# Optimization experiments

Measured on AMD Instinct MI355X. Metric: run time of the kernel, lower is better.

## Reference

```python
import jax, jax.numpy as jnp
import numpy as np

_SAMPLING_EPS = 1e-5
EOS_PROB_RATIO = 100.0
MIN_PROB_THRESHOLD = 0.001
MIX_RATIO = 0.5
EOS_TOKEN_ID = 2


def setup_inputs() -> dict:
    key = jax.random.key(0)
    k1, k2, k3, k4 = jax.random.split(key, 4)
    B, V = 256, 128000
    logits = jax.random.normal(k1, (B, V), dtype=jnp.float32) * 3.0
    # keep temperature away from 0 so the random-sampling path is exercised
    temperature = 0.2 + 1.3 * jax.random.uniform(k2, (B,), dtype=jnp.float32)
    top_p = 0.5 + 0.5 * jax.random.uniform(k3, (B,), dtype=jnp.float32)
    token_lengths = jax.random.randint(k4, (V,), 0, 20).astype(jnp.int32)
    return {
        "logits": logits,
        "temperature": temperature,
        "top_p": top_p,
        "token_lengths": token_lengths,
        "top_k": 50,
    }


def _apply_top_k_top_p(logits, top_k, top_p):
    """vLLM-style: ascending sort, top-k threshold, top-p cumulative mask, scatter back."""
    idx = jnp.argsort(logits, axis=-1)  # ascending
    lsort = jnp.take_along_axis(logits, idx, axis=-1)
    V = logits.shape[-1]
    # top-k: keep only the last top_k (largest) entries
    kth = lsort[:, V - top_k][:, None]
    lsort = jnp.where(lsort < kth, -jnp.inf, lsort)
    # top-p: mask low-cumulative-probability prefix (ascending order)
    probs = jax.nn.softmax(lsort, axis=-1)
    csum = jnp.cumsum(probs, axis=-1)
    pmask = csum <= (1.0 - top_p[:, None])
    pmask = pmask.at[:, -1].set(False)  # always keep the top token
    lsort = jnp.where(pmask, -jnp.inf, lsort)
    # scatter back to original token order
    inv = jnp.argsort(idx, axis=-1)
    return jnp.take_along_axis(lsort, inv, axis=-1)


def _longest_word_sample(logits, token_lengths, k, mix_ratio, eos_token_id):
    topk_logits, topk_idx = jax.lax.top_k(logits, k)  # [B,k]
    prob = jax.nn.softmax(topk_logits, axis=-1)
    lens = token_lengths[jnp.clip(topk_idx, 0, token_lengths.shape[0] - 1)].astype(jnp.float32)
    length_score = jax.nn.softmax(lens, axis=-1)
    mix = (1.0 - mix_ratio) * prob + mix_ratio * length_score
    mix = jnp.where(prob >= MIN_PROB_THRESHOLD, mix, -jnp.inf)
    # EOS threshold rule
    eos_in_topk = (topk_idx == eos_token_id) & jnp.isfinite(topk_logits)
    rows_with_eos = eos_in_topk.any(axis=-1, keepdims=True)
    eos_prob = jnp.sum(prob * eos_in_topk, axis=-1, keepdims=True)
    eos_thresh = jnp.maximum(eos_prob / EOS_PROB_RATIO, 0.005)
    valid = prob >= eos_thresh
    mix = jnp.where(valid | ~rows_with_eos, mix, -jnp.inf)
    best = jnp.argmax(mix, axis=-1)  # [B]
    chosen = jnp.take_along_axis(topk_idx, best[:, None], axis=-1)[:, 0]
    return chosen


def reference(logits, temperature, top_p, token_lengths, top_k):
    greedy = jnp.argmax(logits, axis=-1)
    scaled = logits / temperature[:, None]
    filtered = _apply_top_k_top_p(scaled, top_k, top_p)
    rnd = _longest_word_sample(filtered, token_lengths, top_k, MIX_RATIO, EOS_TOKEN_ID)
    sampled = jnp.where(temperature < _SAMPLING_EPS, greedy, rnd)
    return sampled.astype(jnp.int32)
```

## Files before the change

### kernel.cpp

```cpp
#include <hip/hip_runtime.h>
#include <stdint.h>
#include <math.h>

#define THREADS 1024
#define NWAVES 16
#define NBINS 8192
#define BIN_SHIFT 19
#define CAND_MAX 1536
#define MAXK 64
#define RING 4

__device__ __forceinline__ uint32_t fkey(float f) {
    uint32_t b = __float_as_uint(f);
    return (b & 0x80000000u) ? ~b : (b | 0x80000000u);
}
__device__ __forceinline__ float fval(uint32_t k) {
    uint32_t b = (k & 0x80000000u) ? (k & 0x7FFFFFFFu) : ~k;
    return __uint_as_float(b);
}

__device__ __forceinline__ void gload_lds16(const float* g, uint32_t* lds) {
    __builtin_amdgcn_global_load_lds(
        (const __attribute__((address_space(1))) void*)(const void*)g,
        (__attribute__((address_space(3))) void*)(void*)lds,
        16, 0, 0);
}

__global__ __launch_bounds__(THREADS, 1) void sampler_kernel(
    const float* __restrict__ logits,
    const float* __restrict__ temperature,
    const float* __restrict__ top_p,
    const int* __restrict__ token_lengths,
    const int* __restrict__ top_k_ptr,
    int* __restrict__ out, int V)
{
    const int row  = blockIdx.x;
    const int tid  = threadIdx.x;
    const int lane = tid & 63;
    const int wid  = tid >> 6;
    int K = *top_k_ptr;
    if (K < 1) K = 1;
    if (K > MAXK) K = MAXK;

    __shared__ __align__(16) uint32_t s_stage[NWAVES * RING * 256];
    __shared__ uint32_t s_hist[NBINS];
    __shared__ unsigned long long s_cand[CAND_MAX];
    __shared__ uint32_t s_wsum[NWAVES], s_wtail[NWAVES];
    __shared__ float s_vals[MAXK];
    __shared__ int s_idx[MAXK], s_slot[MAXK];
    __shared__ int s_T, s_cnt;

    for (int i = tid; i < NBINS; i += THREADS) s_hist[i] = 0u;
    if (tid == 0) s_cnt = 0;
    __syncthreads();

    const float* rowbase = logits + (size_t)row * (size_t)V;
    const int NREAL = (V + 255) >> 8;
    const int NITER = (NREAL + NWAVES - 1) / NWAVES;
    const int lastg = V - 4;
    uint32_t* mystage = &s_stage[wid * (RING * 256)];

    #pragma unroll
    for (int k = 0; k < RING - 1; ++k) {
        int ci = wid + NWAVES * k;
        int c  = (ci < NREAL - 1) ? ci : (NREAL - 1);
        int g  = c * 256 + lane * 4;
        g = (g < lastg) ? g : lastg;
        gload_lds16(rowbase + g, mystage + k * 256);
    }
    for (int i = 0; i < NITER; ++i) {
        asm volatile("s_waitcnt vmcnt(2)" ::: "memory");
        const uint32_t* sp = mystage + (i & (RING - 1)) * 256 + lane * 4;
        float4 x = *reinterpret_cast<const float4*>(sp);
        const int g0 = (wid + NWAVES * i) * 256 + lane * 4;
        if (g0 < V) {
            atomicAdd(&s_hist[fkey(x.x) >> BIN_SHIFT], 1u);
            atomicAdd(&s_hist[fkey(x.y) >> BIN_SHIFT], 1u);
            atomicAdd(&s_hist[fkey(x.z) >> BIN_SHIFT], 1u);
            atomicAdd(&s_hist[fkey(x.w) >> BIN_SHIFT], 1u);
        }
        {
            int ci = wid + NWAVES * (i + RING - 1);
            int c  = (ci < NREAL - 1) ? ci : (NREAL - 1);
            int g  = c * 256 + lane * 4;
            g = (g < lastg) ? g : lastg;
            gload_lds16(rowbase + g, mystage + ((i + RING - 1) & (RING - 1)) * 256);
        }
    }
    asm volatile("s_waitcnt vmcnt(0)" ::: "memory");
    __syncthreads();

    const int CH = NBINS / THREADS;
    uint32_t cs = 0;
    {
        const int b0 = tid * CH;
        #pragma unroll
        for (int b = 0; b < CH; ++b) cs += s_hist[b0 + b];
    }
    uint32_t suf = cs;
    #pragma unroll
    for (int off = 1; off < 64; off <<= 1) {
        uint32_t o = __shfl_down(suf, off, 64);
        suf += (lane + off < 64) ? o : 0u;
    }
    if (lane == 0) s_wsum[wid] = suf;
    __syncthreads();
    if (wid == 0 && lane < NWAVES) {
        uint32_t t = s_wsum[lane];
        uint32_t s = t;
        #pragma unroll
        for (int off = 1; off < NWAVES; off <<= 1) {
            uint32_t o = __shfl_down(s, off, 64);
            s += (lane + off < NWAVES) ? o : 0u;
        }
        s_wtail[lane] = s - t;
    }
    __syncthreads();
    {
        uint32_t sufg = suf + s_wtail[wid];
        uint32_t sufn = sufg - cs;
        if (sufg >= (uint32_t)K && sufn < (uint32_t)K) {
            uint32_t acc = sufn;
            int T = tid * CH;
            for (int b = tid * CH + CH - 1; b >= tid * CH; --b) {
                acc += s_hist[b];
                if (acc >= (uint32_t)K) { T = b; break; }
            }
            s_T = T;
        }
    }
    __syncthreads();

    const uint32_t T = (uint32_t)s_T;
    #pragma unroll
    for (int k = 0; k < RING - 1; ++k) {
        int ci = wid + NWAVES * k;
        int c  = (ci < NREAL - 1) ? ci : (NREAL - 1);
        int g  = c * 256 + lane * 4;
        g = (g < lastg) ? g : lastg;
        gload_lds16(rowbase + g, mystage + k * 256);
    }
    for (int i = 0; i < NITER; ++i) {
        asm volatile("s_waitcnt vmcnt(2)" ::: "memory");
        const uint32_t* sp = mystage + (i & (RING - 1)) * 256 + lane * 4;
        float4 x = *reinterpret_cast<const float4*>(sp);
        const int g0 = (wid + NWAVES * i) * 256 + lane * 4;
        if (g0 < V) {
            uint32_t k0;
            k0 = fkey(x.x); if ((k0 >> BIN_SHIFT) >= T) { int p = atomicAdd(&s_cnt, 1); if (p < CAND_MAX) s_cand[p] = ((unsigned long long)k0 << 32) | (uint32_t)~(uint32_t)(g0 + 0); }
            k0 = fkey(x.y); if ((k0 >> BIN_SHIFT) >= T) { int p = atomicAdd(&s_cnt, 1); if (p < CAND_MAX) s_cand[p] = ((unsigned long long)k0 << 32) | (uint32_t)~(uint32_t)(g0 + 1); }
            k0 = fkey(x.z); if ((k0 >> BIN_SHIFT) >= T) { int p = atomicAdd(&s_cnt, 1); if (p < CAND_MAX) s_cand[p] = ((unsigned long long)k0 << 32) | (uint32_t)~(uint32_t)(g0 + 2); }
            k0 = fkey(x.w); if ((k0 >> BIN_SHIFT) >= T) { int p = atomicAdd(&s_cnt, 1); if (p < CAND_MAX) s_cand[p] = ((unsigned long long)k0 << 32) | (uint32_t)~(uint32_t)(g0 + 3); }
        }
        {
            int ci = wid + NWAVES * (i + RING - 1);
            int c  = (ci < NREAL - 1) ? ci : (NREAL - 1);
            int g  = c * 256 + lane * 4;
            g = (g < lastg) ? g : lastg;
            gload_lds16(rowbase + g, mystage + ((i + RING - 1) & (RING - 1)) * 256);
        }
    }
    asm volatile("s_waitcnt vmcnt(0)" ::: "memory");
    __syncthreads();

    const int M = (s_cnt < CAND_MAX) ? s_cnt : CAND_MAX;
    for (int t = tid; t < M; t += THREADS) {
        const unsigned long long mine = s_cand[t];
        int rank = 0;
        for (int j = 0; j < M; ++j) rank += (s_cand[j] > mine) ? 1 : 0;
        if (rank < MAXK) {
            s_idx[rank]  = (int)(~(uint32_t)mine);
            s_vals[rank] = fval((uint32_t)(mine >> 32));
        }
    }
    __syncthreads();

    if (tid >= 64) return;

    const float temp = temperature[row];
    const float tp   = top_p[row];

    const float a0 = s_vals[0] / temp;
    float e = 0.f;
    int myidx = -1;
    if (tid < K) {
        myidx = s_idx[tid];
        e = expf(s_vals[tid] / temp - a0);
    }
    float sum = e;
    #pragma unroll
    for (int off = 1; off < 64; off <<= 1) sum += __shfl_xor(sum, off, 64);
    const float p1 = e / sum;

    float csf = p1;
    #pragma unroll
    for (int off = 1; off < 64; off <<= 1) {
        float o = __shfl_down(csf, off, 64);
        csf += (tid + off < 64) ? o : 0.f;
    }
    const float lim = 1.0f - tp;
    const bool keep = (tid < K) && (tid == 0 || csf > lim);
    const int S = __popcll(__ballot(keep));

    float e2 = (tid < S) ? e : 0.f;
    float sum2 = e2;
    #pragma unroll
    for (int off = 1; off < 64; off <<= 1) sum2 += __shfl_xor(sum2, off, 64);
    const float p2 = e2 / sum2;

    const bool is_eos = (tid < S) && (myidx == 2);
    float eosp = is_eos ? p2 : 0.f;
    #pragma unroll
    for (int off = 1; off < 64; off <<= 1) eosp += __shfl_xor(eosp, off, 64);
    const bool has_eos = (__ballot(is_eos) != 0ull);
    const float eth = fmaxf(eosp / 100.0f, 0.005f);

    if (tid < S) s_slot[tid] = myidx;
    __builtin_amdgcn_wave_barrier();
    if (tid == 0) {
        unsigned long long m0 = 0ull, m1 = 0ull;
        for (int i = 0; i < S; ++i) {
            int id = s_idx[i];
            if (id < 64) m0 |= 1ull << id;
            else if (id < 128) m1 |= 1ull << (id - 64);
        }
        int nxt = 0;
        for (int i = S; i < K; ++i) {
            while ((nxt < 64) ? ((m0 >> nxt) & 1ull) : ((m1 >> (nxt - 64)) & 1ull)) nxt++;
            s_slot[i] = nxt++;
        }
    }
    __builtin_amdgcn_wave_barrier();

    float len = -INFINITY;
    if (tid < K) {
        int id = s_slot[tid];
        id = (id < 0) ? 0 : ((id >= V) ? V - 1 : id);
        len = (float)token_lengths[id];
    }
    float lmax = len;
    #pragma unroll
    for (int off = 1; off < 64; off <<= 1) lmax = fmaxf(lmax, __shfl_xor(lmax, off, 64));
    float el = (tid < K) ? expf(len - lmax) : 0.f;
    float lsum = el;
    #pragma unroll
    for (int off = 1; off < 64; off <<= 1) lsum += __shfl_xor(lsum, off, 64);
    const float ls = el / lsum;

    float mix = -INFINITY;
    if (tid < S) {
        mix = 0.5f * p2 + 0.5f * ls;
        if (!(p2 >= 0.001f)) mix = -INFINITY;
        if (has_eos && !(p2 >= eth)) mix = -INFINITY;
    }
    float bm = mix; int bi = tid;
    #pragma unroll
    for (int off = 1; off < 64; off <<= 1) {
        float om = __shfl_xor(bm, off, 64);
        int   oi = __shfl_xor(bi, off, 64);
        if (om > bm || (om == bm && oi < bi)) { bm = om; bi = oi; }
    }

    if (tid == 0) {
        int chosen = s_slot[bi];
        if (temp < 1e-5f) chosen = s_idx[0];
        out[row] = chosen;
    }
}

extern "C" void kernel_launch(void* const* d_in, const int* in_sizes, int n_in,
                              void* d_out, int out_size, void* d_ws, size_t ws_size,
                              hipStream_t stream) {
    const float* logits        = (const float*)d_in[0];
    const float* temperature   = (const float*)d_in[1];
    const float* top_p         = (const float*)d_in[2];
    const int*   token_lengths = (const int*)d_in[3];
    const int*   top_k_ptr     = (const int*)d_in[4];
    int* outp = (int*)d_out;

    const int B = in_sizes[1];
    const int V = in_sizes[3];

    sampler_kernel<<<B, THREADS, 0, stream>>>(logits, temperature, top_p,
                                              token_lengths, top_k_ptr, outp, V);
}
```

Before: 51.55 us.

## Replace two-pass histogram top-k with single-pass per-thread top-4 plus fallback

Each thread now streams its slice of the row once with batched float4 register loads and keeps a running top-4 (packed key plus index), plus the largest value it discarded. The histogram and candidate selection then work on only 4096 per-thread survivors instead of rescanning the full row. A check compares the discarded maxima against the K-th result and, if any thread dropped a qualifying element, falls back to a full rescan of the row. This removes the second full pass over global memory and the per-element LDS atomics, at the cost of per-element register insertion work and a rare slow path.

```diff
diff --git a/kernel.cpp b/kernel.cpp
--- a/kernel.cpp
+++ b/kernel.cpp
@@ -6,9 +6,9 @@
 #define NWAVES 16
 #define NBINS 8192
 #define BIN_SHIFT 19
-#define CAND_MAX 1536
+#define CAND_MAX 1024
 #define MAXK 64
-#define RING 4
+#define BATCH 16
 
 __device__ __forceinline__ uint32_t fkey(float f) {
     uint32_t b = __float_as_uint(f);
@@ -19,12 +19,19 @@
     return __uint_as_float(b);
 }
 
-__device__ __forceinline__ void gload_lds16(const float* g, uint32_t* lds) {
-    __builtin_amdgcn_global_load_lds(
-        (const __attribute__((address_space(1))) void*)(const void*)g,
-        (__attribute__((address_space(3))) void*)(void*)lds,
-        16, 0, 0);
-}
+#define INS(vf, gidx) do {                                                       \
+    unsigned long long p_ = ((unsigned long long)fkey(vf) << 32)                 \
+                          | (uint32_t)~(uint32_t)(gidx);                         \
+    if (p_ > t3) {                                                               \
+        dmax = (t3 > dmax) ? t3 : dmax;                                          \
+        t3 = p_;                                                                 \
+        if (t3 > t2) { unsigned long long tt_ = t2; t2 = t3; t3 = tt_; }         \
+        if (t2 > t1) { unsigned long long tt_ = t1; t1 = t2; t2 = tt_; }         \
+        if (t1 > t0) { unsigned long long tt_ = t0; t0 = t1; t1 = tt_; }         \
+    } else {                                                                     \
+        dmax = (p_ > dmax) ? p_ : dmax;                                          \
+    }                                                                            \
+} while (0)
 
 __global__ __launch_bounds__(THREADS, 1) void sampler_kernel(
     const float* __restrict__ logits,
@@ -42,7 +49,7 @@
     if (K < 1) K = 1;
     if (K > MAXK) K = MAXK;
 
-    __shared__ __align__(16) uint32_t s_stage[NWAVES * RING * 256];
+    __shared__ unsigned long long s_cand4[THREADS * 4];
     __shared__ uint32_t s_hist[NBINS];
     __shared__ unsigned long long s_cand[CAND_MAX];
     __shared__ uint32_t s_wsum[NWAVES], s_wtail[NWAVES];
@@ -52,42 +59,42 @@
 
     for (int i = tid; i < NBINS; i += THREADS) s_hist[i] = 0u;
     if (tid == 0) s_cnt = 0;
-    __syncthreads();
 
     const float* rowbase = logits + (size_t)row * (size_t)V;
-    const int NREAL = (V + 255) >> 8;
-    const int NITER = (NREAL + NWAVES - 1) / NWAVES;
-    const int lastg = V - 4;
-    uint32_t* mystage = &s_stage[wid * (RING * 256)];
-
-    #pragma unroll
-    for (int k = 0; k < RING - 1; ++k) {
-        int ci = wid + NWAVES * k;
-        int c  = (ci < NREAL - 1) ? ci : (NREAL - 1);
-        int g  = c * 256 + lane * 4;
-        g = (g < lastg) ? g : lastg;
-        gload_lds16(rowbase + g, mystage + k * 256);
-    }
-    for (int i = 0; i < NITER; ++i) {
-        asm volatile("s_waitcnt vmcnt(2)" ::: "memory");
-        const uint32_t* sp = mystage + (i & (RING - 1)) * 256 + lane * 4;
-        float4 x = *reinterpret_cast<const float4*>(sp);
-        const int g0 = (wid + NWAVES * i) * 256 + lane * 4;
-        if (g0 < V) {
-            atomicAdd(&s_hist[fkey(x.x) >> BIN_SHIFT], 1u);
-            atomicAdd(&s_hist[fkey(x.y) >> BIN_SHIFT], 1u);
-            atomicAdd(&s_hist[fkey(x.z) >> BIN_SHIFT], 1u);
-            atomicAdd(&s_hist[fkey(x.w) >> BIN_SHIFT], 1u);
-        }
-        {
-            int ci = wid + NWAVES * (i + RING - 1);
-            int c  = (ci < NREAL - 1) ? ci : (NREAL - 1);
-            int g  = c * 256 + lane * 4;
-            g = (g < lastg) ? g : lastg;
-            gload_lds16(rowbase + g, mystage + ((i + RING - 1) & (RING - 1)) * 256);
-        }
-    }
-    asm volatile("s_waitcnt vmcnt(0)" ::: "memory");
+    const int nv = V >> 2;
+    const float4* rowp = reinterpret_cast<const float4*>(rowbase);
+    const int jmax = nv - 1;
+
+    unsigned long long t0 = 0ull, t1 = 0ull, t2 = 0ull, t3 = 0ull, dmax = 0ull;
+    for (int base = tid; base < nv; base += THREADS * BATCH) {
+        float4 x[BATCH];
+        #pragma unroll
+        for (int b = 0; b < BATCH; ++b) {
+            int j = base + b * THREADS;
+            x[b] = rowp[(j < jmax) ? j : jmax];
+        }
+        #pragma unroll
+        for (int b = 0; b < BATCH; ++b) {
+            const int j = base + b * THREADS;
+            if (j < nv) {
+                const int g = j << 2;
+                INS(x[b].x, g + 0);
+                INS(x[b].y, g + 1);
+                INS(x[b].z, g + 2);
+                INS(x[b].w, g + 3);
+            }
+        }
+    }
+    __syncthreads();
+
+    s_cand4[tid * 4 + 0] = t0;
+    s_cand4[tid * 4 + 1] = t1;
+    s_cand4[tid * 4 + 2] = t2;
+    s_cand4[tid * 4 + 3] = t3;
+    atomicAdd(&s_hist[(uint32_t)(t0 >> 32) >> BIN_SHIFT], 1u);
+    atomicAdd(&s_hist[(uint32_t)(t1 >> 32) >> BIN_SHIFT], 1u);
+    atomicAdd(&s_hist[(uint32_t)(t2 >> 32) >> BIN_SHIFT], 1u);
+    atomicAdd(&s_hist[(uint32_t)(t3 >> 32) >> BIN_SHIFT], 1u);
     __syncthreads();
 
     const int CH = NBINS / THREADS;
@@ -133,34 +140,13 @@
 
     const uint32_t T = (uint32_t)s_T;
     #pragma unroll
-    for (int k = 0; k < RING - 1; ++k) {
-        int ci = wid + NWAVES * k;
-        int c  = (ci < NREAL - 1) ? ci : (NREAL - 1);
-        int g  = c * 256 + lane * 4;
-        g = (g < lastg) ? g : lastg;
-        gload_lds16(rowbase + g, mystage + k * 256);
-    }
-    for (int i = 0; i < NITER; ++i) {
-        asm volatile("s_waitcnt vmcnt(2)" ::: "memory");
-        const uint32_t* sp = mystage + (i & (RING - 1)) * 256 + lane * 4;
-        float4 x = *reinterpret_cast<const float4*>(sp);
-        const int g0 = (wid + NWAVES * i) * 256 + lane * 4;
-        if (g0 < V) {
-            uint32_t k0;
-            k0 = fkey(x.x); if ((k0 >> BIN_SHIFT) >= T) { int p = atomicAdd(&s_cnt, 1); if (p < CAND_MAX) s_cand[p] = ((unsigned long long)k0 << 32) | (uint32_t)~(uint32_t)(g0 + 0); }
-            k0 = fkey(x.y); if ((k0 >> BIN_SHIFT) >= T) { int p = atomicAdd(&s_cnt, 1); if (p < CAND_MAX) s_cand[p] = ((unsigned long long)k0 << 32) | (uint32_t)~(uint32_t)(g0 + 1); }
-            k0 = fkey(x.z); if ((k0 >> BIN_SHIFT) >= T) { int p = atomicAdd(&s_cnt, 1); if (p < CAND_MAX) s_cand[p] = ((unsigned long long)k0 << 32) | (uint32_t)~(uint32_t)(g0 + 2); }
-            k0 = fkey(x.w); if ((k0 >> BIN_SHIFT) >= T) { int p = atomicAdd(&s_cnt, 1); if (p < CAND_MAX) s_cand[p] = ((unsigned long long)k0 << 32) | (uint32_t)~(uint32_t)(g0 + 3); }
-        }
-        {
-            int ci = wid + NWAVES * (i + RING - 1);
-            int c  = (ci < NREAL - 1) ? ci : (NREAL - 1);
-            int g  = c * 256 + lane * 4;
-            g = (g < lastg) ? g : lastg;
-            gload_lds16(rowbase + g, mystage + ((i + RING - 1) & (RING - 1)) * 256);
-        }
-    }
-    asm volatile("s_waitcnt vmcnt(0)" ::: "memory");
+    for (int r = 0; r < 4; ++r) {
+        unsigned long long c = s_cand4[tid * 4 + r];
+        if (((uint32_t)(c >> 32) >> BIN_SHIFT) >= T) {
+            int p = atomicAdd(&s_cnt, 1);
+            if (p < CAND_MAX) s_cand[p] = c;
+        }
+    }
     __syncthreads();
 
     const int M = (s_cnt < CAND_MAX) ? s_cnt : CAND_MAX;
@@ -174,6 +160,35 @@
         }
     }
     __syncthreads();
+
+    const unsigned long long kth =
+        ((unsigned long long)fkey(s_vals[K - 1]) << 32)
+        | (uint32_t)~(uint32_t)s_idx[K - 1];
+    const int bad = (dmax > kth) ? 1 : 0;
+    if (__syncthreads_or(bad)) {
+        if (tid == 0) s_cnt = 0;
+        __syncthreads();
+        for (int j = tid; j < V; j += THREADS) {
+            unsigned long long p = ((unsigned long long)fkey(rowbase[j]) << 32)
+                                 | (uint32_t)~(uint32_t)j;
+            if (p >= kth) {
+                int q = atomicAdd(&s_cnt, 1);
+                if (q < CAND_MAX) s_cand[q] = p;
+            }
+        }
+        __syncthreads();
+        const int M2 = (s_cnt < CAND_MAX) ? s_cnt : CAND_MAX;
+        for (int t = tid; t < M2; t += THREADS) {
+            const unsigned long long mine = s_cand[t];
+            int rank = 0;
+            for (int j = 0; j < M2; ++j) rank += (s_cand[j] > mine) ? 1 : 0;
+            if (rank < MAXK) {
+                s_idx[rank]  = (int)(~(uint32_t)mine);
+                s_vals[rank] = fval((uint32_t)(mine >> 32));
+            }
+        }
+        __syncthreads();
+    }
 
     if (tid >= 64) return;
 
```

New measurement: 64.02 us. +24.2%, slower.
